# Kernel optimization log

Measured on AMD Instinct MI355X. Metric: run time of the kernel, lower is better.

## Reference

```python
import jax, jax.numpy as jnp
import numpy as np

B, N, DIM, H = 2, 2048, 1024, 16
D = DIM // H  # head_dim = 64


def setup_inputs() -> dict:
    key = jax.random.key(0)
    ks = jax.random.split(key, 3)
    w_scale = 0.02
    return {
        "x": jax.random.normal(ks[0], (B, N, DIM), dtype=jnp.float32),
        "Wqkv": jax.random.normal(ks[1], (DIM, 3 * DIM), dtype=jnp.float32) * w_scale,
        "bqkv": jnp.zeros((3 * DIM,), dtype=jnp.float32),
        "Wproj": jax.random.normal(ks[2], (DIM, DIM), dtype=jnp.float32) * w_scale,
        "bproj": jnp.zeros((DIM,), dtype=jnp.float32),
        "sigma": jnp.ones((1,), dtype=jnp.float32),
        "gamma": jnp.ones((1,), dtype=jnp.float32),
    }


def reference(x, Wqkv, bqkv, Wproj, bproj, sigma, gamma):
    b, n, c = x.shape
    # qkv projection -> (B, N, 3, H, D)
    qkv = (x @ Wqkv + bqkv).reshape(b, n, 3, H, D)
    q = jnp.transpose(qkv[:, :, 0], (0, 2, 1, 3))  # [B, H, N, D]
    k = jnp.transpose(qkv[:, :, 1], (0, 2, 1, 3))
    v = jnp.transpose(qkv[:, :, 2], (0, 2, 1, 3))
    scale = 1.0 / jnp.sqrt(jnp.asarray(D, dtype=x.dtype))
    scores = jnp.einsum("bhqd,bhkd->bhqk", q, k) * scale  # [B, H, N, N]
    # divisive normalization (cortical gain control) over key axis
    denom = sigma + jnp.sqrt(jnp.mean(scores * scores, axis=-1, keepdims=True))
    scores = gamma * scores / denom
    attn = jax.nn.softmax(scores, axis=-1)
    out = jnp.einsum("bhqk,bhkd->bhqd", attn, v)  # [B, H, N, D]
    out = jnp.transpose(out, (0, 2, 1, 3)).reshape(b, n, c)
    return out @ Wproj + bproj
```

## Files before the change

### kernel.cpp

```cpp
#include <hip/hip_runtime.h>

typedef __attribute__((ext_vector_type(4))) float f32x4;
typedef __attribute__((ext_vector_type(8))) _Float16 f16x8;
typedef __attribute__((ext_vector_type(4))) _Float16 f16x4;
typedef __attribute__((ext_vector_type(2))) _Float16 f16x2;

#define MFMA_F16(a, b, c) __builtin_amdgcn_mfma_f32_16x16x32_f16(a, b, c, 0, 0, 0)

__device__ __forceinline__ void gload_lds16(const void* g, void* l) {
  __builtin_amdgcn_global_load_lds(
      (const __attribute__((address_space(1))) void*)g,
      (__attribute__((address_space(3))) void*)l, 16, 0, 0);
}
__device__ __forceinline__ f16x2 pk2(float a, float b) {
  return __builtin_bit_cast(f16x2, __builtin_amdgcn_cvt_pkrtz(a, b));
}
__device__ __forceinline__ void pipe_barrier_v4() {
  asm volatile("s_waitcnt vmcnt(4) lgkmcnt(0)" ::: "memory");
  __builtin_amdgcn_sched_barrier(0);
  __builtin_amdgcn_s_barrier();
}
__device__ __forceinline__ void pipe_barrier_v3() {
  asm volatile("s_waitcnt vmcnt(3) lgkmcnt(0)" ::: "memory");
  __builtin_amdgcn_sched_barrier(0);
  __builtin_amdgcn_s_barrier();
}
__device__ __forceinline__ void pipe_barrier_v2() {
  asm volatile("s_waitcnt vmcnt(2) lgkmcnt(0)" ::: "memory");
  __builtin_amdgcn_sched_barrier(0);
  __builtin_amdgcn_s_barrier();
}
__device__ __forceinline__ void pipe_barrier_v0() {
  asm volatile("s_waitcnt vmcnt(0) lgkmcnt(0)" ::: "memory");
  __builtin_amdgcn_sched_barrier(0);
  __builtin_amdgcn_s_barrier();
}

__global__ __launch_bounds__(256) void prep_kernel(
    const float* __restrict__ x, _Float16* __restrict__ xf,
    const float* __restrict__ Wqkv, _Float16* __restrict__ wqt,
    const float* __restrict__ Wproj, _Float16* __restrict__ wpt) {
  __shared__ float tile[32][33];
  const int bx = blockIdx.x;
  if (bx < 4096) {
    const int i = bx * 256 + threadIdx.x;
    f32x4 v = *(const f32x4*)(x + (size_t)i * 4);
    f16x4 h;
#pragma unroll
    for (int j = 0; j < 4; ++j) h[j] = (_Float16)v[j];
    *(f16x4*)(xf + (size_t)i * 4) = h;
    return;
  }
  const float* W;
  _Float16* wt;
  int N, n0, k0;
  if (bx < 7168) {
    const int t = bx - 4096;
    W = Wqkv; wt = wqt; N = 3072;
    n0 = (t % 96) * 32; k0 = (t / 96) * 32;
  } else {
    const int t = bx - 7168;
    W = Wproj; wt = wpt; N = 1024;
    n0 = (t % 32) * 32; k0 = (t / 32) * 32;
  }
  const int tx = threadIdx.x & 31, ty = threadIdx.x >> 5;
#pragma unroll
  for (int j = 0; j < 32; j += 8)
    tile[ty + j][tx] = W[(size_t)(k0 + ty + j) * N + n0 + tx];
  __syncthreads();
#pragma unroll
  for (int j = 0; j < 32; j += 8)
    wt[(size_t)(n0 + ty + j) * 1024 + k0 + tx] = (_Float16)tile[tx][ty + j];
}

__global__ __launch_bounds__(256) void gemm_qkv_kernel(
    const _Float16* __restrict__ xf, const _Float16* __restrict__ wt,
    const float* __restrict__ bias, _Float16* __restrict__ QF,
    _Float16* __restrict__ KF, _Float16* __restrict__ KT,
    _Float16* __restrict__ VT) {
  __shared__ __attribute__((aligned(16))) _Float16 lg[24576];
  const int tid = threadIdx.x, lane = tid & 63, w = tid >> 6;
  const int wg = blockIdx.x;
  const int cx = wg & 7, c = wg >> 3;
  const int bxl = (cx & 1) * 12 + c % 12;
  const int byl = (cx >> 1) * 8 + c / 12;
  const int m0 = byl * 128, n0 = bxl * 128;
  const int wr = (w >> 1) * 64, wc = (w & 1) * 64;
  f32x4 acc[4][4] = {};

  const int srow = lane >> 2;
  const int scol = (((lane & 3) ^ ((lane >> 3) & 3)) * 8);
  const int fr = lane & 15, fg = lane >> 4;
  const int rswz = (fr >> 1) & 3;

  auto stageT = [&](int buf, int k0) {
#pragma unroll
    for (int j = 0; j < 2; ++j) {
      const int rbase = 32 * w + 16 * j;
      const int r = rbase + srow;
      gload_lds16(xf + (size_t)(m0 + r) * 1024 + k0 + scol,
                  &lg[buf * 8192 + rbase * 32]);
      gload_lds16(wt + (size_t)(n0 + r) * 1024 + k0 + scol,
                  &lg[buf * 8192 + 4096 + rbase * 32]);
    }
  };

  stageT(0, 0);
  stageT(1, 32);
  pipe_barrier_v4();
  int cur = 0;
  for (int t = 0; t < 32; ++t) {
    if (t < 30) {
      const int nb = (cur + 2 >= 3) ? cur - 1 : cur + 2;
      stageT(nb, (t + 2) * 32);
    }
    const int ab = cur * 8192;
    f16x8 af[4], bfr[4];
#pragma unroll
    for (int m = 0; m < 4; ++m)
      af[m] = *(const f16x8*)&lg[ab + (wr + 16 * m + fr) * 32 + ((fg ^ rswz) * 8)];
#pragma unroll
    for (int n = 0; n < 4; ++n)
      bfr[n] = *(const f16x8*)&lg[ab + 4096 + (wc + 16 * n + fr) * 32 + ((fg ^ rswz) * 8)];
#pragma unroll
    for (int m = 0; m < 4; ++m)
#pragma unroll
      for (int n = 0; n < 4; ++n) acc[m][n] = MFMA_F16(af[m], bfr[n], acc[m][n]);
    if (t < 30) pipe_barrier_v4(); else pipe_barrier_v0();
    cur = (cur + 1 == 3) ? 0 : cur + 1;
  }

  const int fq = fg * 4;
#pragma unroll
  for (int n = 0; n < 4; ++n) {
    const float bv = bias[n0 + wc + 16 * n + fr];
#pragma unroll
    for (int m = 0; m < 4; ++m)
#pragma unroll
      for (int i = 0; i < 4; ++i)
        lg[(wr + 16 * m + fq + i) * 129 + wc + 16 * n + fr] =
            (_Float16)(acc[m][n][i] + bv);
  }
  __syncthreads();
  const int b = m0 >> 11, nnb = m0 & 2047;
  const int h0 = 2 * (bxl & 7);
  const int sPhase = bxl >> 3;
  if (sPhase <= 1) {
    _Float16* __restrict__ dst = (sPhase == 0) ? QF : KF;
#pragma unroll
    for (int p = 0; p < 8; ++p) {
      const int r = p * 16 + (tid >> 4);
      const int cc = tid & 15;
      f16x8 vals;
#pragma unroll
      for (int j = 0; j < 8; ++j) vals[j] = lg[r * 129 + cc * 8 + j];
      const int h = cc >> 3, d = (cc & 7) * 8;
      *(f16x8*)&dst[((size_t)((b * 16 + h0 + h) * 2048 + nnb + r)) * 64 + d] = vals;
    }
  }
  if (sPhase >= 1) {
    _Float16* __restrict__ T = (sPhase == 1) ? KT : VT;
#pragma unroll
    for (int p = 0; p < 8; ++p) {
      const int lr = p * 16 + (tid >> 4);
      const int cc = tid & 15;
      f16x8 vals;
#pragma unroll
      for (int j = 0; j < 8; ++j) vals[j] = lg[(cc * 8 + j) * 129 + lr];
      const int h = lr >> 6, d = lr & 63;
      *(f16x8*)&T[((size_t)((b * 16 + h0 + h) * 64 + d)) * 2048 + nnb + cc * 8] = vals;
    }
  }
}

__global__ __launch_bounds__(256) void gram_partial_kernel(
    const _Float16* __restrict__ KT, float* __restrict__ GP) {
  __shared__ __attribute__((aligned(16))) _Float16 sT[3][4096];
  const int tid = threadIdx.x, lane = tid & 63, w = tid >> 6;
  const int bh = blockIdx.x >> 2, qt = blockIdx.x & 3;
  const _Float16* src = KT + (size_t)bh * 64 * 2048 + qt * 512;
  const int s_r = lane >> 3, s_cg = lane & 7;
  const int fr = lane & 15, fg = lane >> 4;
  const int kswz = fr & 7;

  auto stage = [&](int buf, int n0) {
#pragma unroll
    for (int j = 0; j < 2; ++j) {
      const int rbase = 8 * w + 32 * j;
      gload_lds16(src + (size_t)(rbase + s_r) * 2048 + n0 + ((s_cg ^ s_r) * 8),
                  &sT[buf][rbase * 64]);
    }
  };

  f32x4 acc[4] = {};
  stage(0, 0);
  stage(1, 64);
  pipe_barrier_v2();
  int cur = 0;
  for (int t = 0; t < 8; ++t) {
    if (t < 6) {
      const int nb = (cur + 2 >= 3) ? cur - 1 : cur + 2;
      stage(nb, (t + 2) * 64);
    }
    f16x8 af[2];
#pragma unroll
    for (int ks = 0; ks < 2; ++ks)
      af[ks] = *(const f16x8*)&sT[cur][(16 * w + fr) * 64 + (((ks * 4 + fg) ^ kswz) * 8)];
#pragma unroll
    for (int nt = 0; nt < 4; ++nt)
#pragma unroll
      for (int ks = 0; ks < 2; ++ks)
        acc[nt] = MFMA_F16(
            af[ks],
            *(const f16x8*)&sT[cur][(16 * nt + fr) * 64 + (((ks * 4 + fg) ^ kswz) * 8)],
            acc[nt]);
    if (t < 6) pipe_barrier_v2(); else pipe_barrier_v0();
    cur = (cur + 1 == 3) ? 0 : cur + 1;
  }
  float* dst = GP + (size_t)blockIdx.x * 4096;
#pragma unroll
  for (int nt = 0; nt < 4; ++nt)
#pragma unroll
    for (int i = 0; i < 4; ++i)
      dst[(16 * w + fg * 4 + i) * 64 + 16 * nt + fr] = acc[nt][i];
}

__global__ __launch_bounds__(256) void gram_reduce_kernel(
    const float* __restrict__ GP, _Float16* __restrict__ GH,
    _Float16* __restrict__ GL) {
  const int bh = blockIdx.x >> 2, seg = blockIdx.x & 3;
  const int e0 = seg * 1024 + threadIdx.x * 4;
  const float* p = GP + (size_t)bh * 4 * 4096 + e0;
  f32x4 s = *(const f32x4*)p;
  s += *(const f32x4*)(p + 4096);
  s += *(const f32x4*)(p + 8192);
  s += *(const f32x4*)(p + 12288);
  f16x4 gh, gl;
#pragma unroll
  for (int j = 0; j < 4; ++j) {
    gh[j] = (_Float16)s[j];
    gl[j] = (_Float16)(s[j] - (float)gh[j]);
  }
  *(f16x4*)&GH[(size_t)bh * 4096 + e0] = gh;
  *(f16x4*)&GL[(size_t)bh * 4096 + e0] = gl;
}

__global__ __launch_bounds__(256) void attn_kernel(
    const _Float16* __restrict__ QF, const _Float16* __restrict__ KF,
    const _Float16* __restrict__ VT, const _Float16* __restrict__ GH,
    const _Float16* __restrict__ GL, _Float16* __restrict__ OB,
    const float* __restrict__ sigma_p, const float* __restrict__ gamma_p) {
  __shared__ __attribute__((aligned(16))) _Float16 lds[24576];

  const int tid = threadIdx.x, lane = tid & 63, w = tid >> 6;
  const int wg = blockIdx.x;
  const int c = wg >> 3;
  const int bh = (wg & 7) * 4 + (c >> 4);
  const int q0 = (c & 15) * 128;
  const size_t base = (size_t)bh * (2048 * 64);
  const float sigma = sigma_p[0], gamma = gamma_p[0];
  const int fr = lane & 15, fg = lane >> 4;
  const int s_r = lane >> 3, s_cg = lane & 7;
  const int kswz = fr & 7;

  const _Float16* Kbh = KF + base;
  const _Float16* Tbh = VT + base;

  f16x8 qf[2][2];
#pragma unroll
  for (int m = 0; m < 2; ++m)
#pragma unroll
    for (int ks = 0; ks < 2; ++ks)
      qf[m][ks] = *(const f16x8*)(QF + base +
                                  (size_t)(q0 + 32 * w + 16 * m + fr) * 64 +
                                  ks * 32 + fg * 8);

  auto stage64 = [&](int dstoff, const _Float16* g, int srcstride) {
#pragma unroll
    for (int j = 0; j < 2; ++j) {
      const int rbase = 8 * w + 32 * j;
      gload_lds16(g + (size_t)(rbase + s_r) * srcstride + ((s_cg ^ s_r) * 8),
                  &lds[dstoff + rbase * 64]);
    }
  };
  auto stage64K = [&](int dstoff, const _Float16* g) {
#pragma unroll
    for (int j = 0; j < 2; ++j) {
      const int rbase = 8 * w + 32 * j;
      const int r = rbase + s_r;
      const int pr = (r & 0x23) | ((r & 0x0C) << 1) | ((r & 0x10) >> 2);
      gload_lds16(g + (size_t)pr * 64 + ((s_cg ^ s_r) * 8),
                  &lds[dstoff + rbase * 64]);
    }
  };

  stage64(0, GH + (size_t)bh * 4096, 64);
  stage64(4096, GL + (size_t)bh * 4096, 64);
  __syncthreads();
  float minvl2[2];
  float* Yp = (float*)&lds[8192 + w * 2048];
#pragma unroll
  for (int m = 0; m < 2; ++m) {
    f32x4 yacc[4] = {};
#pragma unroll
    for (int nt = 0; nt < 4; ++nt) {
#pragma unroll
      for (int ks = 0; ks < 2; ++ks) {
        const int off = (16 * nt + fr) * 64 + (((ks * 4 + fg) ^ kswz) * 8);
        yacc[nt] = MFMA_F16(qf[m][ks], *(const f16x8*)&lds[off], yacc[nt]);
        yacc[nt] = MFMA_F16(qf[m][ks], *(const f16x8*)&lds[4096 + off], yacc[nt]);
      }
    }
#pragma unroll
    for (int nt = 0; nt < 4; ++nt)
#pragma unroll
      for (int i = 0; i < 4; ++i) Yp[(fg * 4 + i) * 64 + 16 * nt + fr] = yacc[nt][i];
    float zp = 0.0f;
#pragma unroll
    for (int ks = 0; ks < 2; ++ks) {
      const f32x4 y0 = *(const f32x4*)&Yp[fr * 64 + ks * 32 + fg * 8];
      const f32x4 y1 = *(const f32x4*)&Yp[fr * 64 + ks * 32 + fg * 8 + 4];
#pragma unroll
      for (int cc = 0; cc < 4; ++cc) {
        zp += y0[cc] * (float)qf[m][ks][cc];
        zp += y1[cc] * (float)qf[m][ks][cc + 4];
      }
    }
    zp += __shfl_xor(zp, 16);
    zp += __shfl_xor(zp, 32);
    const float rms = sqrtf(fmaxf(zp, 0.0f)) * (1.0f / 362.038672f);
    minvl2[m] = gamma / (sigma + rms) * 0.125f * 1.44269504f;
  }
  __syncthreads();

  float lsum[2] = {};
  f32x4 oacc[2][4] = {};

  auto qk_tile = [&](int kbuf, f32x4 (&pn)[2][4]) {
#pragma unroll
    for (int n = 0; n < 4; ++n) {
      const int offb = kbuf * 4096 + (16 * n + fr) * 64;
      const f16x8 kf0 = *(const f16x8*)&lds[offb + ((fg ^ kswz) * 8)];
      const f16x8 kf1 = *(const f16x8*)&lds[offb + (((4 + fg) ^ kswz) * 8)];
#pragma unroll
      for (int m = 0; m < 2; ++m) {
        f32x4 a = {};
        a = MFMA_F16(kf0, qf[m][0], a);
        a = MFMA_F16(kf1, qf[m][1], a);
        pn[m][n] = a;
      }
    }
  };
  auto exp_pack = [&](f32x4 (&pn)[2][4], f16x8 (&pa)[2][2]) {
#pragma unroll
    for (int m = 0; m < 2; ++m) {
#pragma unroll
      for (int n = 0; n < 4; ++n)
#pragma unroll
        for (int i = 0; i < 4; ++i) {
          const float p = __builtin_amdgcn_exp2f(pn[m][n][i] * minvl2[m]);
          lsum[m] += p;
          pn[m][n][i] = p;
        }
#pragma unroll
      for (int k2 = 0; k2 < 2; ++k2) {
        const f16x2 c0 = pk2(pn[m][2 * k2][0], pn[m][2 * k2][1]);
        const f16x2 c1 = pk2(pn[m][2 * k2][2], pn[m][2 * k2][3]);
        const f16x2 c2 = pk2(pn[m][2 * k2 + 1][0], pn[m][2 * k2 + 1][1]);
        const f16x2 c3 = pk2(pn[m][2 * k2 + 1][2], pn[m][2 * k2 + 1][3]);
        pa[m][k2][0] = c0[0]; pa[m][k2][1] = c0[1];
        pa[m][k2][2] = c1[0]; pa[m][k2][3] = c1[1];
        pa[m][k2][4] = c2[0]; pa[m][k2][5] = c2[1];
        pa[m][k2][6] = c3[0]; pa[m][k2][7] = c3[1];
      }
    }
  };
  auto pv_tile = [&](int vbuf, f16x8 (&pa)[2][2]) {
#pragma unroll
    for (int k2 = 0; k2 < 2; ++k2) {
#pragma unroll
      for (int nf = 0; nf < 4; ++nf) {
        const int off = 12288 + vbuf * 4096 + (16 * nf + fr) * 64 +
                        (((k2 * 4 + fg) ^ kswz) * 8);
        const f16x8 vt = *(const f16x8*)&lds[off];
        oacc[0][nf] = MFMA_F16(vt, pa[0][k2], oacc[0][nf]);
        oacc[1][nf] = MFMA_F16(vt, pa[1][k2], oacc[1][nf]);
      }
    }
  };

  stage64K(0, Kbh);
  stage64(12288, Tbh, 2048);
  stage64K(4096, Kbh + 4096);
  stage64(16384, Tbh + 64, 2048);
  pipe_barrier_v0();

  f32x4 pn[2][4];
  f16x8 pa[2][2], pan[2][2];
  qk_tile(0, pn);
  exp_pack(pn, pa);

  for (int t = 0; t < 32; ++t) {
    const int cb = t % 3;
    if (t < 30) {
      const int sb = (t + 2) % 3;
      stage64K(sb * 4096, Kbh + (size_t)(t + 2) * 4096);
      stage64(12288 + sb * 4096, Tbh + (t + 2) * 64, 2048);
    }
    if (t < 31) {
      __builtin_amdgcn_s_setprio(1);
      qk_tile((t + 1) % 3, pn);
      __builtin_amdgcn_s_setprio(0);
    }
    __builtin_amdgcn_s_setprio(1);
    pv_tile(cb, pa);
    __builtin_amdgcn_s_setprio(0);
    if (t < 31) {
      exp_pack(pn, pan);
#pragma unroll
      for (int m = 0; m < 2; ++m)
#pragma unroll
        for (int k2 = 0; k2 < 2; ++k2) pa[m][k2] = pan[m][k2];
      pipe_barrier_v0();
    }
  }

  float inv[2];
#pragma unroll
  for (int m = 0; m < 2; ++m) {
    lsum[m] += __shfl_xor(lsum[m], 16);
    lsum[m] += __shfl_xor(lsum[m], 32);
    inv[m] = 1.0f / lsum[m];
  }

  const int b = bh >> 4, h = bh & 15;
#pragma unroll
  for (int m = 0; m < 2; ++m) {
    const size_t orow = (size_t)(b * 2048 + q0 + 32 * w + 16 * m + fr);
#pragma unroll
    for (int nf = 0; nf < 4; ++nf) {
      f16x4 ov;
#pragma unroll
      for (int i = 0; i < 4; ++i) ov[i] = (_Float16)(oacc[m][nf][i] * inv[m]);
      *(f16x4*)&OB[orow * 1024 + h * 64 + 16 * nf + 4 * fg] = ov;
    }
  }
}

__global__ __launch_bounds__(256) void gemm_proj_kernel(
    const _Float16* __restrict__ A, const _Float16* __restrict__ Bt,
    const float* __restrict__ bias, float* __restrict__ out) {
  __shared__ __attribute__((aligned(16))) _Float16 lg[18432];
  const int tid = threadIdx.x, lane = tid & 63, w = tid >> 6;
  const int wg = blockIdx.x;
  const int c = wg >> 3;
  const int bxl = c & 7;
  const int byl = (wg & 7) * 8 + (c >> 3);
  const int m0 = byl * 64, n0 = bxl * 128;
  const int wr = (w >> 1) * 32, wc = (w & 1) * 64;
  f32x4 acc[2][4] = {};
  const int srow = lane >> 2;
  const int scol = (((lane & 3) ^ ((lane >> 3) & 3)) * 8);
  const int fr = lane & 15, fg = lane >> 4;
  const int rswz = (fr >> 1) & 3;

  auto stageT = [&](int buf, int k0) {
    {
      const int rbase = 16 * w;
      gload_lds16(A + (size_t)(m0 + rbase + srow) * 1024 + k0 + scol,
                  &lg[buf * 6144 + rbase * 32]);
    }
#pragma unroll
    for (int j = 0; j < 2; ++j) {
      const int rbase = 32 * w + 16 * j;
      gload_lds16(Bt + (size_t)(n0 + rbase + srow) * 1024 + k0 + scol,
                  &lg[buf * 6144 + 2048 + rbase * 32]);
    }
  };

  stageT(0, 0);
  stageT(1, 32);
  pipe_barrier_v3();
  int cur = 0;
  for (int t = 0; t < 32; ++t) {
    if (t < 30) {
      const int nb = (cur + 2 >= 3) ? cur - 1 : cur + 2;
      stageT(nb, (t + 2) * 32);
    }
    const int ab = cur * 6144;
    f16x8 af[2], bfr[4];
#pragma unroll
    for (int m = 0; m < 2; ++m)
      af[m] = *(const f16x8*)&lg[ab + (wr + 16 * m + fr) * 32 + ((fg ^ rswz) * 8)];
#pragma unroll
    for (int n = 0; n < 4; ++n)
      bfr[n] = *(const f16x8*)&lg[ab + 2048 + (wc + 16 * n + fr) * 32 + ((fg ^ rswz) * 8)];
#pragma unroll
    for (int m = 0; m < 2; ++m)
#pragma unroll
      for (int n = 0; n < 4; ++n) acc[m][n] = MFMA_F16(af[m], bfr[n], acc[m][n]);
    if (t < 30) pipe_barrier_v3(); else pipe_barrier_v0();
    cur = (cur + 1 == 3) ? 0 : cur + 1;
  }
  const int fq = fg * 4;
#pragma unroll
  for (int n = 0; n < 4; ++n) {
    const int col = n0 + wc + 16 * n + fr;
    const float bv = bias[col];
#pragma unroll
    for (int m = 0; m < 2; ++m) {
#pragma unroll
      for (int i = 0; i < 4; ++i) {
        const int row = m0 + wr + 16 * m + fq + i;
        out[(size_t)row * 1024 + col] = acc[m][n][i] + bv;
      }
    }
  }
}

extern "C" void kernel_launch(void* const* d_in, const int* in_sizes, int n_in,
                              void* d_out, int out_size, void* d_ws, size_t ws_size,
                              hipStream_t stream) {
  const float* x = (const float*)d_in[0];
  const float* Wqkv = (const float*)d_in[1];
  const float* bqkv = (const float*)d_in[2];
  const float* Wproj = (const float*)d_in[3];
  const float* bproj = (const float*)d_in[4];
  const float* sigma = (const float*)d_in[5];
  const float* gamma = (const float*)d_in[6];
  float* out = (float*)d_out;

  char* ws = (char*)d_ws;
  const size_t MB = 1024 * 1024;
  _Float16* XF  = (_Float16*)(ws + 0 * MB);
  _Float16* WQT = (_Float16*)(ws + 8 * MB);
  _Float16* WPT = (_Float16*)(ws + 14 * MB);
  _Float16* QF  = (_Float16*)(ws + 16 * MB);
  _Float16* KF  = (_Float16*)(ws + 24 * MB);
  _Float16* VT  = (_Float16*)(ws + 32 * MB);
  _Float16* KT  = (_Float16*)(ws + 40 * MB);
  _Float16* OB  = (_Float16*)(ws + 40 * MB);
  _Float16* GH  = (_Float16*)(ws + 8 * MB);
  _Float16* GL  = (_Float16*)(ws + 8 * MB + 512 * 1024);
  float*    GP  = (float*)(ws + 9 * MB);

  prep_kernel<<<8192, 256, 0, stream>>>(x, XF, Wqkv, WQT, Wproj, WPT);
  gemm_qkv_kernel<<<768, 256, 0, stream>>>(XF, WQT, bqkv, QF, KF, KT, VT);
  gram_partial_kernel<<<128, 256, 0, stream>>>(KT, GP);
  gram_reduce_kernel<<<128, 256, 0, stream>>>(GP, GH, GL);
  attn_kernel<<<512, 256, 0, stream>>>(QF, KF, VT, GH, GL, OB, sigma, gamma);
  gemm_proj_kernel<<<512, 256, 0, stream>>>(OB, WPT, bproj, out);
}
```

Before: 124.6 us.

## Deepen K/V staging to four LDS buffers with partial vmcnt waits

Moves the attention loop's K/V staging from a triple buffer to a quad buffer, prefetching three tiles ahead. The per-iteration barrier now waits only until the oldest loads finish (vmcnt(4)) instead of draining every outstanding global load. The loop is also unrolled by two with ping-pong P registers, which removes the register copy. The aim is to hide global-load latency behind the MFMA work. In exchange, LDS use grows from 48KB to 64KB per block, which may lower occupancy.

```diff
diff --git a/kernel.cpp b/kernel.cpp
--- a/kernel.cpp
+++ b/kernel.cpp
@@ -32,6 +32,11 @@
 }
 __device__ __forceinline__ void pipe_barrier_v0() {
   asm volatile("s_waitcnt vmcnt(0) lgkmcnt(0)" ::: "memory");
+  __builtin_amdgcn_sched_barrier(0);
+  __builtin_amdgcn_s_barrier();
+}
+__device__ __forceinline__ void wait_barrier_v4() {
+  asm volatile("s_waitcnt vmcnt(4) lgkmcnt(0)" ::: "memory");
   __builtin_amdgcn_sched_barrier(0);
   __builtin_amdgcn_s_barrier();
 }
@@ -250,7 +255,7 @@
     const _Float16* __restrict__ VT, const _Float16* __restrict__ GH,
     const _Float16* __restrict__ GL, _Float16* __restrict__ OB,
     const float* __restrict__ sigma_p, const float* __restrict__ gamma_p) {
-  __shared__ __attribute__((aligned(16))) _Float16 lds[24576];
+  __shared__ __attribute__((aligned(16))) _Float16 lds[32768];
 
   const int tid = threadIdx.x, lane = tid & 63, w = tid >> 6;
   const int wg = blockIdx.x;
@@ -293,6 +298,10 @@
                   &lds[dstoff + rbase * 64]);
     }
   };
+  auto stage_tile = [&](int b, int kb) {
+    stage64K(b * 4096, Kbh + (size_t)kb * 4096);
+    stage64(16384 + b * 4096, Tbh + kb * 64, 2048);
+  };
 
   stage64(0, GH + (size_t)bh * 4096, 64);
   stage64(4096, GL + (size_t)bh * 4096, 64);
@@ -380,7 +389,7 @@
     for (int k2 = 0; k2 < 2; ++k2) {
 #pragma unroll
       for (int nf = 0; nf < 4; ++nf) {
-        const int off = 12288 + vbuf * 4096 + (16 * nf + fr) * 64 +
+        const int off = 16384 + vbuf * 4096 + (16 * nf + fr) * 64 +
                         (((k2 * 4 + fg) ^ kswz) * 8);
         const f16x8 vt = *(const f16x8*)&lds[off];
         oacc[0][nf] = MFMA_F16(vt, pa[0][k2], oacc[0][nf]);
@@ -389,40 +398,34 @@
     }
   };
 
-  stage64K(0, Kbh);
-  stage64(12288, Tbh, 2048);
-  stage64K(4096, Kbh + 4096);
-  stage64(16384, Tbh + 64, 2048);
-  pipe_barrier_v0();
-
   f32x4 pn[2][4];
-  f16x8 pa[2][2], pan[2][2];
-  qk_tile(0, pn);
-  exp_pack(pn, pa);
-
-  for (int t = 0; t < 32; ++t) {
-    const int cb = t % 3;
-    if (t < 30) {
-      const int sb = (t + 2) % 3;
-      stage64K(sb * 4096, Kbh + (size_t)(t + 2) * 4096);
-      stage64(12288 + sb * 4096, Tbh + (t + 2) * 64, 2048);
-    }
+  f16x8 paA[2][2], paB[2][2];
+
+  auto body = [&](int t, f16x8 (&paIn)[2][2], f16x8 (&paOut)[2][2]) {
+    if (t < 29) stage_tile((t + 3) & 3, t + 3);
     if (t < 31) {
       __builtin_amdgcn_s_setprio(1);
-      qk_tile((t + 1) % 3, pn);
+      qk_tile((t + 1) & 3, pn);
       __builtin_amdgcn_s_setprio(0);
     }
     __builtin_amdgcn_s_setprio(1);
-    pv_tile(cb, pa);
+    pv_tile(t & 3, paIn);
     __builtin_amdgcn_s_setprio(0);
-    if (t < 31) {
-      exp_pack(pn, pan);
-#pragma unroll
-      for (int m = 0; m < 2; ++m)
-#pragma unroll
-        for (int k2 = 0; k2 < 2; ++k2) pa[m][k2] = pan[m][k2];
-      pipe_barrier_v0();
-    }
+    if (t < 31) exp_pack(pn, paOut);
+    if (t < 29) pipe_barrier_v4();
+    else if (t < 31) pipe_barrier_v0();
+  };
+
+  stage_tile(0, 0);
+  stage_tile(1, 1);
+  stage_tile(2, 2);
+  wait_barrier_v4();
+  qk_tile(0, pn);
+  exp_pack(pn, paA);
+
+  for (int t = 0; t < 32; t += 2) {
+    body(t, paA, paB);
+    body(t + 1, paB, paA);
   }
 
   float inv[2];
```

After: 123.2 us. No clear change (-1.1%).
